# Optimization experiments

Hardware: AMD Instinct MI355X
Metric: run time of the kernel (lower is better)

Reference implementation:

```python
import jax, jax.numpy as jnp
import numpy as np

B, T, S = 32, 1000, 100
D, A, H, E, V, P = 512, 1024, 1024, 640, 10240, 1024
ZH, ZC = 0.05, 0.15  # zoneout factors (eval-mode deterministic blend)
NEG = -1e30


def setup_inputs() -> dict:
    key = jax.random.key(0)
    ks = jax.random.split(key, 20)
    w = lambda k, shape, s=0.02: jax.random.normal(k, shape, jnp.float32) * s
    return {
        "encoder_outputs": jax.random.normal(ks[0], (B, T, D), jnp.float32),
        "labels": jax.random.randint(ks[1], (B, S), 0, V),
        "enc_seq_len": jax.random.randint(ks[2], (B,), T // 2, T + 1).astype(jnp.int32),
        "embed": w(ks[3], (V, E)),
        "W_ih": w(ks[4], (4 * H, E + D)),
        "W_hh": w(ks[5], (4 * H, H)),
        "b_ih": jnp.zeros((4 * H,), jnp.float32),
        "b_hh": jnp.zeros((4 * H,), jnp.float32),
        "W_s": w(ks[6], (A, H)),
        "W_enc": w(ks[7], (A, D)),
        "b_enc": jnp.zeros((A,), jnp.float32),
        "v_att": w(ks[8], (1, A)),
        "W_fert": w(ks[9], (1, D)),
        "W_fb": w(ks[10], (A, 1)),
        "W_ro": w(ks[11], (P, H + E + D)),
        "b_ro": jnp.zeros((P,), jnp.float32),
        "W_out": w(ks[12], (V, P // 2)),
        "b_out": jnp.zeros((V,), jnp.float32),
    }


def _decoder(encoder_outputs, labels, enc_seq_len, embed, W_ih, W_hh, b_ih, b_hh,
             W_s, W_enc, b_enc, v_att, W_fert, W_fb, W_ro, b_ro, W_out, b_out):
    Bb, Tt, Dd = encoder_outputs.shape
    Hh = W_hh.shape[1]
    # shifted target embeddings (BOS = zeros): [B,S,E]
    emb = embed[labels]
    emb = jnp.pad(emb, ((0, 0), (1, 0), (0, 0)))[:, :-1, :]
    enc_ctx = jnp.einsum('btd,ad->bta', encoder_outputs, W_enc) + b_enc      # [B,T,A]
    inv_fert = jax.nn.sigmoid(jnp.einsum('btd,od->bto', encoder_outputs, W_fert))  # [B,T,1]
    mask = (jnp.arange(Tt)[None, :] < enc_seq_len[:, None])[:, :, None]      # [B,T,1]

    def step(carry, emb_t):
        h, c, att_ctx, accum = carry
        x = jnp.concatenate([emb_t, att_ctx], axis=-1)                       # [B,E+D]
        gates = x @ W_ih.T + b_ih + h @ W_hh.T + b_hh                        # [B,4H]
        i, f, g, o = jnp.split(gates, 4, axis=-1)
        c_new = jax.nn.sigmoid(f) * c + jax.nn.sigmoid(i) * jnp.tanh(g)
        h_new = jax.nn.sigmoid(o) * jnp.tanh(c_new)
        # zoneout (eval-mode expectation)
        h = ZH * h + (1.0 - ZH) * h_new
        c = ZC * c + (1.0 - ZC) * c_new
        s_t = h @ W_s.T                                                      # [B,A]
        fb = accum @ W_fb.T                                                  # [B,T,1]@[1,A] -> [B,T,A]
        energies = jnp.tanh(enc_ctx + s_t[:, None, :] + fb) @ v_att.T        # [B,T,1]
        energies = jnp.where(mask, energies, NEG)
        w_att = jax.nn.softmax(energies, axis=1)                             # [B,T,1]
        ctx = jnp.einsum('bt,btd->bd', w_att[..., 0], encoder_outputs)       # [B,D]
        accum = accum + w_att * inv_fert * 0.5
        return (h, c, ctx, accum), (h, ctx)

    zeros_h = jnp.zeros((Bb, Hh), encoder_outputs.dtype)
    carry0 = (zeros_h, zeros_h,
              jnp.zeros((Bb, Dd), encoder_outputs.dtype),
              jnp.zeros((Bb, Tt, 1), encoder_outputs.dtype))
    _, (s_seq, ctx_seq) = jax.lax.scan(step, carry0, jnp.swapaxes(emb, 0, 1))
    s_stk = jnp.swapaxes(s_seq, 0, 1)        # [B,S,H]
    ctx_stk = jnp.swapaxes(ctx_seq, 0, 1)    # [B,S,D]
    ro = jnp.concatenate([s_stk, emb, ctx_stk], axis=-1) @ W_ro.T + b_ro     # [B,S,P]
    ro = ro.reshape(ro.shape[0], ro.shape[1], -1, 2).max(axis=-1)            # MaxOut -> [B,S,P/2]
    logits = ro @ W_out.T + b_out                                            # [B,S,V]
    return logits


def reference(encoder_outputs, labels, enc_seq_len, embed, W_ih, W_hh, b_ih, b_hh,
              W_s, W_enc, b_enc, v_att, W_fert, W_fb, W_ro, b_ro, W_out, b_out):
    return _decoder(encoder_outputs, labels, enc_seq_len, embed, W_ih, W_hh, b_ih, b_hh,
                    W_s, W_enc, b_enc, v_att, W_fert, W_fb, W_ro, b_ro, W_out, b_out)
```

## Files before the change

### kernel.cpp

```cpp
#include <hip/hip_runtime.h>
#include <hip/hip_bf16.h>

typedef __bf16 bf16x8 __attribute__((ext_vector_type(8)));
typedef __bf16 bf16x4 __attribute__((ext_vector_type(4)));
typedef float  f32x4  __attribute__((ext_vector_type(4)));
typedef unsigned long long u64;

#define DI __device__ __forceinline__

DI float ex2f_(float x){ return __builtin_amdgcn_exp2f(x); }
DI float rcpf_(float x){ return __builtin_amdgcn_rcpf(x); }

DI u64 cload64(const void* p){
  return __hip_atomic_load((const u64*)p, __ATOMIC_RELAXED, __HIP_MEMORY_SCOPE_AGENT);
}
DI float cloadf(const float* p){
  return __hip_atomic_load(p, __ATOMIC_RELAXED, __HIP_MEMORY_SCOPE_AGENT);
}
DI void cstoreu(unsigned* p, unsigned v){
  __hip_atomic_store(p, v, __ATOMIC_RELAXED, __HIP_MEMORY_SCOPE_AGENT);
}
DI void cstoref(float* p, float v){
  __hip_atomic_store(p, v, __ATOMIC_RELAXED, __HIP_MEMORY_SCOPE_AGENT);
}

DI void bar_sync(unsigned* cnt, unsigned* flag, unsigned target){
  __syncthreads();
  if (threadIdx.x == 0){
    asm volatile("s_waitcnt vmcnt(0) lgkmcnt(0)" ::: "memory");
    __builtin_amdgcn_sched_barrier(0);
    unsigned old = __hip_atomic_fetch_add(cnt, 1u, __ATOMIC_RELAXED, __HIP_MEMORY_SCOPE_AGENT);
    if (old == target - 1u){
      __hip_atomic_store(flag, 1u, __ATOMIC_RELAXED, __HIP_MEMORY_SCOPE_AGENT);
    } else {
      while (__hip_atomic_load(flag, __ATOMIC_RELAXED, __HIP_MEMORY_SCOPE_AGENT) == 0u){
        __builtin_amdgcn_s_sleep(2);
      }
    }
    __builtin_amdgcn_sched_barrier(0);
  }
  __syncthreads();
}


__global__ void f32_to_bf16_k(const float* __restrict__ src, __bf16* __restrict__ dst, int n4){
  int i = blockIdx.x*256 + threadIdx.x;
  if (i >= n4) return;
  float4 v = reinterpret_cast<const float4*>(src)[i];
  bf16x4 o; o[0]=(__bf16)v.x; o[1]=(__bf16)v.y; o[2]=(__bf16)v.z; o[3]=(__bf16)v.w;
  reinterpret_cast<bf16x4*>(dst)[i] = o;
}

__global__ void emb_gather_k(const float* __restrict__ embed, const int* __restrict__ labels,
                             __bf16* __restrict__ out){
  int i = blockIdx.x*256 + threadIdx.x;
  if (i >= 100*32*80) return;
  int e8 = (i % 80)*8;
  int g  = i / 80;
  int b  = g & 31, s = g >> 5;
  bf16x8 o;
  if (s == 0){
    #pragma unroll
    for (int u=0;u<8;u++) o[u] = (__bf16)0.f;
  } else {
    int lbl = labels[b*100 + (s-1)];
    const float* pe = embed + (size_t)lbl*640 + e8;
    #pragma unroll
    for (int u=0;u<8;u++) o[u] = (__bf16)pe[u];
  }
  *reinterpret_cast<bf16x8*>(out + (size_t)g*640 + e8) = o;
}

__global__ __launch_bounds__(256) void fert_k(const float* __restrict__ enc,
                       const float* __restrict__ Wf, float* __restrict__ inv_fert){
  int row  = blockIdx.x*4 + (threadIdx.x>>6);
  int lane = threadIdx.x & 63;
  const float* pr = enc + (size_t)row*512 + lane*8;
  const float* pw = Wf + lane*8;
  float4 a0 = reinterpret_cast<const float4*>(pr)[0];
  float4 a1 = reinterpret_cast<const float4*>(pr)[1];
  float4 w0 = reinterpret_cast<const float4*>(pw)[0];
  float4 w1 = reinterpret_cast<const float4*>(pw)[1];
  float acc = a0.x*w0.x + a0.y*w0.y + a0.z*w0.z + a0.w*w0.w
            + a1.x*w1.x + a1.y*w1.y + a1.z*w1.z + a1.w*w1.w;
  #pragma unroll
  for (int off=1; off<64; off<<=1) acc += __shfl_xor(acc, off, 64);
  if (lane == 0) inv_fert[row] = 1.f/(1.f + expf(-acc));
}

__global__ void init_k(float* h, float* c, __bf16* hb, float* ctx_un, float* accum,
                       float* expe, float* sumb, unsigned* bars){
  int i = blockIdx.x*256 + threadIdx.x;
  if (i < 32768){ h[i]=0.f; c[i]=0.f; hb[i]=(__bf16)0.f; }
  if (i < 16384) ctx_un[i]=0.f;
  if (i < 32000) accum[i]=0.f;
  if (i < 64000) expe[i]=0.f;
  if (i < 64)    sumb[i]=1.f;
  if (i < 8192)  bars[i]=0u;
}

template<int MODE>
__global__ __launch_bounds__(256) void gemm_bt(const __bf16* __restrict__ A0,
        const __bf16* __restrict__ A1, const __bf16* __restrict__ A2,
        const __bf16* __restrict__ Bw, const float* __restrict__ bias,
        float* __restrict__ outF, __bf16* __restrict__ outB, int M, int N, int K){
  __shared__ __bf16 lA[64][40];
  __shared__ __bf16 lB[64][40];
  const int m0 = blockIdx.x*64, n0 = blockIdx.y*64;
  const int tid = threadIdx.x;
  const int wave = tid>>6, lane = tid&63;
  const int wm = wave>>1, wn = wave&1;
  const int srow = tid>>2, sc8 = (tid&3)*8;
  f32x4 acc[2][2];
  #pragma unroll
  for (int a=0;a<2;a++)
    #pragma unroll
    for (int b2=0;b2<2;b2++){ acc[a][b2][0]=0.f; acc[a][b2][1]=0.f; acc[a][b2][2]=0.f; acc[a][b2][3]=0.f; }

  for (int k0 = 0; k0 < K; k0 += 32){
    const int kk = k0 + sc8;
    bf16x8 av, bv;
    if (MODE == 1){
      const int m = m0 + srow;
      if (kk < 1024)      av = *reinterpret_cast<const bf16x8*>(A0 + (size_t)m*1024 + kk);
      else if (kk < 1664) av = *reinterpret_cast<const bf16x8*>(A1 + (size_t)m*640 + (kk-1024));
      else                av = *reinterpret_cast<const bf16x8*>(A2 + (size_t)m*512 + (kk-1664));
    } else {
      av = *reinterpret_cast<const bf16x8*>(A0 + (size_t)(m0+srow)*K + kk);
    }
    bv = *reinterpret_cast<const bf16x8*>(Bw + (size_t)(n0+srow)*K + kk);
    __syncthreads();
    *reinterpret_cast<bf16x8*>(&lA[srow][sc8]) = av;
    *reinterpret_cast<bf16x8*>(&lB[srow][sc8]) = bv;
    __syncthreads();
    #pragma unroll
    for (int mt=0;mt<2;mt++){
      bf16x8 af = *reinterpret_cast<const bf16x8*>(&lA[wm*32+mt*16+(lane&15)][(lane>>4)*8]);
      #pragma unroll
      for (int nt=0;nt<2;nt++){
        bf16x8 bf = *reinterpret_cast<const bf16x8*>(&lB[wn*32+nt*16+(lane&15)][(lane>>4)*8]);
        acc[mt][nt] = __builtin_amdgcn_mfma_f32_16x16x32_bf16(af, bf, acc[mt][nt], 0,0,0);
      }
    }
  }
  #pragma unroll
  for (int mt=0;mt<2;mt++){
    #pragma unroll
    for (int nt=0;nt<2;nt++){
      #pragma unroll
      for (int r=0;r<4;r++){
        const int m = m0 + wm*32 + mt*16 + (lane>>4)*4 + r;
        const int n = n0 + wn*32 + nt*16 + (lane&15);
        float v = acc[mt][nt][r] + bias[n];
        if (MODE == 0){
          outB[(size_t)m*N + n] = (__bf16)v;
        } else if (MODE == 1){
          float vo = fmaxf(v, __shfl_xor(v, 1, 64));
          if ((lane & 1) == 0) outB[(size_t)m*512 + (n>>1)] = (__bf16)vo;
        } else {
          const int rr = (m & 31)*100 + (m >> 5);
          outF[(size_t)rr*N + n] = v;
        }
      }
    }
  }
}

struct DecArgs {
  const float* b_ih; const float* b_hh;
  const float* v_att; const float* W_fb;
  const int* seqlen;
  const float* inv_fert;
  const __bf16* emb_sbe;
  const __bf16* W_ih_b; const __bf16* W_hh_b; const __bf16* W_s_b;
  const __bf16* enc_ctx; const __bf16* enc_b16;
  float* h_st; float* c_st; __bf16* h_b16;
  float* s_t; float* ctx_un; float* sum_buf;
  float* accum; float* expe;
  __bf16* s_stk; __bf16* ctx_stk;
  unsigned* bars;
};

struct SPd {
  __bf16 hA[32][1032];
  __bf16 cxA[32][520];
  float red[8][2][16][16];
  float gbuf[32][16];
  float sums[32];
};
struct SQd {
  __bf16 hb[1024];
  float st[1024];
  float she[128];
  float invp;
  float cred[8][516];
};

__global__ __launch_bounds__(512, 1) void decoder_kernel(DecArgs g){
  __shared__ __align__(16) char smem_raw[sizeof(SPd)];
  SPd& sp = *reinterpret_cast<SPd*>(smem_raw);
  SQd& sq = *reinterpret_cast<SQd*>(smem_raw);
  const int blk = blockIdx.x, tid = threadIdx.x;
  const int wave = tid>>6, lane = tid&63;
  const int bb = blk & 31, tc = blk >> 5;
  unsigned* bflag = g.bars + 4096;

  for (int s = 0; s < 100; ++s){
    const int p = s & 1, pp = 1 - p;

    {
      if (tid < 32) sp.sums[tid] = 1.f / cloadf(g.sum_buf + pp*32 + tid);
      __syncthreads();
      #pragma unroll
      for (int it = 0; it < 16; ++it){
        int i = tid + it*512;
        int row = i >> 8, c4 = (i & 255) * 4;
        *reinterpret_cast<u64*>(&sp.hA[row][c4]) = cload64(g.h_b16 + row*1024 + c4);
      }
      #pragma unroll
      for (int it = 0; it < 16; ++it){
        int i = tid + it*512;
        int row = i >> 8, c2 = (i & 255) * 2;
        u64 v = cload64(g.ctx_un + row*512 + c2);
        float2 f = __builtin_bit_cast(float2, v);
        float inv = sp.sums[row];
        __bf16 b0 = (__bf16)(f.x * inv), b1 = (__bf16)(f.y * inv);
        unsigned u = (unsigned)__builtin_bit_cast(unsigned short, b0)
                   | ((unsigned)__builtin_bit_cast(unsigned short, b1) << 16);
        *reinterpret_cast<unsigned*>(&sp.cxA[row][c2]) = u;
      }
      __syncthreads();

      const int j0 = blk*4;
      const int c = lane & 15, kg = lane >> 4;
      const int n = ((c>>2)<<10) + j0 + (c&3);
      const int brow0 = c, brow1 = c + 16;
      const int s0   = (wave<4) ? wave*9 : 36 + (wave-4)*8;
      const int scnt = (wave<4) ? 9 : 8;
      f32x4 acc0, acc1;
      acc0[0]=acc0[1]=acc0[2]=acc0[3]=0.f;
      acc1[0]=acc1[1]=acc1[2]=acc1[3]=0.f;
      const __bf16* embS = g.emb_sbe + (size_t)s*32*640;
      for (int ks = s0; ks < s0 + scnt; ++ks){
        const int kk = ks*32 + kg*8;
        bf16x8 bfrag = (kk < 1152)
          ? *reinterpret_cast<const bf16x8*>(g.W_ih_b + (size_t)n*1152 + kk)
          : *reinterpret_cast<const bf16x8*>(g.W_hh_b + (size_t)n*1024 + (kk-1152));
        bf16x8 a0, a1;
        if (kk < 640){
          a0 = *reinterpret_cast<const bf16x8*>(embS + brow0*640 + kk);
          a1 = *reinterpret_cast<const bf16x8*>(embS + brow1*640 + kk);
        } else if (kk < 1152){
          a0 = *reinterpret_cast<const bf16x8*>(&sp.cxA[brow0][kk-640]);
          a1 = *reinterpret_cast<const bf16x8*>(&sp.cxA[brow1][kk-640]);
        } else {
          a0 = *reinterpret_cast<const bf16x8*>(&sp.hA[brow0][kk-1152]);
          a1 = *reinterpret_cast<const bf16x8*>(&sp.hA[brow1][kk-1152]);
        }
        acc0 = __builtin_amdgcn_mfma_f32_16x16x32_bf16(a0, bfrag, acc0, 0,0,0);
        acc1 = __builtin_amdgcn_mfma_f32_16x16x32_bf16(a1, bfrag, acc1, 0,0,0);
      }
      #pragma unroll
      for (int r=0;r<4;r++){
        sp.red[wave][0][kg*4+r][c] = acc0[r];
        sp.red[wave][1][kg*4+r][c] = acc1[r];
      }
      __syncthreads();
      {
        const int mt = tid>>8, row = (tid>>4)&15, col = tid&15;
        float v = 0.f;
        #pragma unroll
        for (int w=0;w<8;w++) v += sp.red[w][mt][row][col];
        const int n2 = ((col>>2)<<10) + j0 + (col&3);
        sp.gbuf[mt*16+row][col] = v + g.b_ih[n2] + g.b_hh[n2];
      }
      __syncthreads();
      if (tid < 64){
        const int b = tid>>1, u = tid&1;
        unsigned packed = 0;
        #pragma unroll
        for (int d=0; d<2; ++d){
          const int cb = 2*u + d;
          const int j = j0 + cb;
          const float gi = sp.gbuf[b][cb],   gf = sp.gbuf[b][4+cb];
          const float gg = sp.gbuf[b][8+cb], go = sp.gbuf[b][12+cb];
          const float c_old = g.c_st[b*1024+j], h_old = g.h_st[b*1024+j];
          const float si = 1.f/(1.f+expf(-gi));
          const float sf = 1.f/(1.f+expf(-gf));
          const float so = 1.f/(1.f+expf(-go));
          const float cn = sf*c_old + si*tanhf(gg);
          const float hn = so*tanhf(cn);
          const float hz = 0.05f*h_old + 0.95f*hn;
          const float cz = 0.15f*c_old + 0.85f*cn;
          g.c_st[b*1024+j] = cz;
          g.h_st[b*1024+j] = hz;
          __bf16 hb = (__bf16)hz;
          packed |= ((unsigned)__builtin_bit_cast(unsigned short, hb)) << (16*d);
        }
        cstoreu(reinterpret_cast<unsigned*>(g.h_b16 + b*1024 + j0 + 2*u), packed);
        *reinterpret_cast<unsigned*>(g.s_stk + ((size_t)s*32+b)*1024 + j0 + 2*u) = packed;
      }
    }
    bar_sync(g.bars + s, bflag + s, 256);

    {
      if (tid < 256){
        *reinterpret_cast<u64*>(&sq.hb[tid*4]) = cload64(g.h_b16 + bb*1024 + tid*4);
      }
      if (tid == 500) sq.invp = 1.f / cloadf(g.sum_buf + pp*32 + bb);
      __syncthreads();
      const float invp = sq.invp;
      {
        const int a = tc*128 + (tid>>2), kc = tid&3;
        const __bf16* wr = g.W_s_b + (size_t)a*1024 + kc*256;
        const __bf16* hr = &sq.hb[kc*256];
        float acc = 0.f;
        #pragma unroll
        for (int i=0;i<32;i++){
          bf16x8 w8 = *reinterpret_cast<const bf16x8*>(wr + i*8);
          bf16x8 h8 = *reinterpret_cast<const bf16x8*>(hr + i*8);
          #pragma unroll
          for (int u2=0;u2<8;u2++) acc = fmaf((float)w8[u2], (float)h8[u2], acc);
        }
        acc += __shfl_xor(acc, 1, 64);
        acc += __shfl_xor(acc, 2, 64);
        if (kc == 0) cstoref(g.s_t + bb*1024 + a, acc);
      }
      if (tid < 64){
        const int d = tc*64 + tid;
        if (s > 0){
          const float cv = cloadf(g.ctx_un + bb*512 + d);
          g.ctx_stk[((size_t)(s-1)*32+bb)*512 + d] = (__bf16)(cv * invp);
        }
        cstoref(g.ctx_un + bb*512 + d, 0.f);
      }
      if (tid < 125){
        const int t = tc*125 + tid, idx = bb*1000 + t;
        g.accum[idx] = fmaf(g.expe[pp*32000+idx]*g.inv_fert[idx], 0.5f*invp, g.accum[idx]);
      }
      if (tid == 501 && tc == 0) cstoref(g.sum_buf + p*32 + bb, 0.f);
    }
    bar_sync(g.bars + 200 + s*32 + bb, bflag + 200 + s*32 + bb, 8);

    {
      const int t_base = tc*125;
      *reinterpret_cast<u64*>(&sq.st[tid*2]) = cload64(g.s_t + bb*1024 + tid*2);
      __syncthreads();
      const int len_b = g.seqlen[bb];
      float sv[16], v2[16], wf[16];
      float vbase = 0.f;
      #pragma unroll
      for (int half=0; half<2; ++half){
        const int a0i = half*512 + lane*8;
        const float4 sA = *reinterpret_cast<const float4*>(&sq.st[a0i]);
        const float4 sB = *reinterpret_cast<const float4*>(&sq.st[a0i+4]);
        const float4 vA = *reinterpret_cast<const float4*>(g.v_att + a0i);
        const float4 vB = *reinterpret_cast<const float4*>(g.v_att + a0i + 4);
        const float4 fA = *reinterpret_cast<const float4*>(g.W_fb + a0i);
        const float4 fB = *reinterpret_cast<const float4*>(g.W_fb + a0i + 4);
        sv[half*8+0]=sA.x; sv[half*8+1]=sA.y; sv[half*8+2]=sA.z; sv[half*8+3]=sA.w;
        sv[half*8+4]=sB.x; sv[half*8+5]=sB.y; sv[half*8+6]=sB.z; sv[half*8+7]=sB.w;
        wf[half*8+0]=fA.x; wf[half*8+1]=fA.y; wf[half*8+2]=fA.z; wf[half*8+3]=fA.w;
        wf[half*8+4]=fB.x; wf[half*8+5]=fB.y; wf[half*8+6]=fB.z; wf[half*8+7]=fB.w;
        v2[half*8+0]=-2.f*vA.x; v2[half*8+1]=-2.f*vA.y; v2[half*8+2]=-2.f*vA.z; v2[half*8+3]=-2.f*vA.w;
        v2[half*8+4]=-2.f*vB.x; v2[half*8+5]=-2.f*vB.y; v2[half*8+6]=-2.f*vB.z; v2[half*8+7]=-2.f*vB.w;
        vbase += vA.x+vA.y+vA.z+vA.w+vB.x+vB.y+vB.z+vB.w;
      }
      float wsum = 0.f;
      {
        const __bf16* ebase = g.enc_ctx + ((size_t)bb*1000)*1024 + lane*8;
        const int nIter = (wave < 5) ? 16 : 15;
        int t = t_base + wave;
        bf16x8 curA = *reinterpret_cast<const bf16x8*>(ebase + (size_t)t*1024);
        bf16x8 curB = *reinterpret_cast<const bf16x8*>(ebase + (size_t)t*1024 + 512);
        for (int k = 0; k < nIter; ++k){
          const int tn = t + 8;
          bf16x8 nxtA = curA, nxtB = curB;
          if (k + 1 < nIter){
            nxtA = *reinterpret_cast<const bf16x8*>(ebase + (size_t)tn*1024);
            nxtB = *reinterpret_cast<const bf16x8*>(ebase + (size_t)tn*1024 + 512);
          }
          const int idx = bb*1000 + t;
          float px = 0.f;
          if (t < len_b){
            const float ac = g.accum[idx];
            float e = vbase;
            #pragma unroll
            for (int u=0;u<8;u++){
              const float z = fmaf(ac, wf[u], sv[u] + (float)curA[u]);
              e = fmaf(v2[u], rcpf_(ex2f_(z * 2.885390082f) + 1.f), e);
            }
            #pragma unroll
            for (int u=0;u<8;u++){
              const float z = fmaf(ac, wf[8+u], sv[8+u] + (float)curB[u]);
              e = fmaf(v2[8+u], rcpf_(ex2f_(z * 2.885390082f) + 1.f), e);
            }
            #pragma unroll
            for (int off=1; off<64; off<<=1) e += __shfl_xor(e, off, 64);
            px = ex2f_(e * 1.44269504f);
          }
          if (lane == 0){
            g.expe[p*32000 + idx] = px;
            sq.she[t - t_base] = px;
          }
          wsum += px;
          curA = nxtA; curB = nxtB;
          t = tn;
        }
      }
      if (lane == 0) atomicAdd(g.sum_buf + p*32 + bb, wsum);
      __syncthreads();
      {
        const int d8 = (tid & 63) * 8;
        const int tt = wave;
        float cacc[8];
        #pragma unroll
        for (int u=0;u<8;u++) cacc[u] = 0.f;
        const __bf16* vb = g.enc_b16 + ((size_t)bb*1000)*512 + d8;
        const int nI2 = (tt < 5) ? 16 : 15;
        int t2 = t_base + tt;
        #pragma unroll 4
        for (int k = 0; k < nI2; ++k){
          const float w = sq.she[t2 - t_base];
          const bf16x8 ev = *reinterpret_cast<const bf16x8*>(vb + (size_t)t2*512);
          #pragma unroll
          for (int u=0;u<8;u++) cacc[u] = fmaf(w, (float)ev[u], cacc[u]);
          t2 += 8;
        }
        #pragma unroll
        for (int u=0;u<8;u++) sq.cred[tt][d8+u] = cacc[u];
        __syncthreads();
        const int d = tid & 511;
        float ssum = 0.f;
        #pragma unroll
        for (int w8=0; w8<8; ++w8) ssum += sq.cred[w8][d];
        atomicAdd(g.ctx_un + bb*512 + d, ssum);
      }
    }
    bar_sync(g.bars + 100 + s, bflag + 100 + s, 256);
  }

  if (tid < 64){
    const int d = tc*64 + tid;
    const float invp = 1.f / cloadf(g.sum_buf + 32 + bb);
    const float cv = cloadf(g.ctx_un + bb*512 + d);
    g.ctx_stk[((size_t)99*32 + bb)*512 + d] = (__bf16)(cv * invp);
  }
}

extern "C" void kernel_launch(void* const* d_in, const int* in_sizes, int n_in,
                              void* d_out, int out_size, void* d_ws, size_t ws_size,
                              hipStream_t stream){
  (void)in_sizes; (void)n_in; (void)out_size; (void)ws_size;
  const float* enc    = (const float*)d_in[0];
  const int*   labels = (const int*)  d_in[1];
  const int*   seqlen = (const int*)  d_in[2];
  const float* embed  = (const float*)d_in[3];
  const float* W_ih   = (const float*)d_in[4];
  const float* W_hh   = (const float*)d_in[5];
  const float* b_ih   = (const float*)d_in[6];
  const float* b_hh   = (const float*)d_in[7];
  const float* W_s    = (const float*)d_in[8];
  const float* W_enc  = (const float*)d_in[9];
  const float* b_enc  = (const float*)d_in[10];
  const float* v_att  = (const float*)d_in[11];
  const float* W_fert = (const float*)d_in[12];
  const float* W_fb   = (const float*)d_in[13];
  const float* W_ro   = (const float*)d_in[14];
  const float* b_ro   = (const float*)d_in[15];
  const float* W_out  = (const float*)d_in[16];
  const float* b_out  = (const float*)d_in[17];
  float* out = (float*)d_out;

  char* ws = (char*)d_ws;
  size_t off = 0;
  auto alloc = [&](size_t bytes)->char*{
    char* p = ws + off;
    off = (off + bytes + 255) & ~(size_t)255;
    return p;
  };
  __bf16* enc_b16 = (__bf16*)alloc(32000ull*512*2);
  __bf16* enc_ctx = (__bf16*)alloc(32000ull*1024*2);
  __bf16* W_ih_b  = (__bf16*)alloc(4096ull*1152*2);
  __bf16* W_hh_b  = (__bf16*)alloc(4096ull*1024*2);
  __bf16* W_s_b   = (__bf16*)alloc(1024ull*1024*2);
  __bf16* W_enc_b = (__bf16*)alloc(1024ull*512*2);
  __bf16* W_ro_b  = (__bf16*)alloc(1024ull*2176*2);
  __bf16* W_out_b = (__bf16*)alloc(10240ull*512*2);
  __bf16* emb_sbe = (__bf16*)alloc(3200ull*640*2);
  float*  ifert   = (float*)alloc(32000ull*4);
  __bf16* s_stk   = (__bf16*)alloc(3200ull*1024*2);
  __bf16* ctx_stk = (__bf16*)alloc(3200ull*512*2);
  float*  h_st    = (float*)alloc(32768ull*4);
  float*  c_st    = (float*)alloc(32768ull*4);
  __bf16* h_b16   = (__bf16*)alloc(32768ull*2);
  float*  s_t     = (float*)alloc(32768ull*4);
  float*  ctx_un  = (float*)alloc(16384ull*4);
  float*  sum_buf = (float*)alloc(256);
  float*  accum   = (float*)alloc(32000ull*4);
  float*  expe    = (float*)alloc(64000ull*4);
  __bf16* Y       = (__bf16*)alloc(3200ull*512*2);
  unsigned* bars  = (unsigned*)alloc(8192ull*4);

  auto conv = [&](const float* s, __bf16* d, int n){
    int n4 = n/4;
    f32_to_bf16_k<<<(n4+255)/256, 256, 0, stream>>>(s, d, n4);
  };
  conv(enc,   enc_b16, 32000*512);
  conv(W_ih,  W_ih_b,  4096*1152);
  conv(W_hh,  W_hh_b,  4096*1024);
  conv(W_s,   W_s_b,   1024*1024);
  conv(W_enc, W_enc_b, 1024*512);
  conv(W_ro,  W_ro_b,  1024*2176);
  conv(W_out, W_out_b, 10240*512);

  emb_gather_k<<<(256000+255)/256, 256, 0, stream>>>(embed, labels, emb_sbe);
  fert_k<<<8000, 256, 0, stream>>>(enc, W_fert, ifert);
  init_k<<<250, 256, 0, stream>>>(h_st, c_st, h_b16, ctx_un, accum, expe, sum_buf, bars);

  gemm_bt<0><<<dim3(500,16), 256, 0, stream>>>(enc_b16, nullptr, nullptr, W_enc_b,
        b_enc, nullptr, enc_ctx, 32000, 1024, 512);

  DecArgs da;
  da.b_ih = b_ih; da.b_hh = b_hh; da.v_att = v_att; da.W_fb = W_fb;
  da.seqlen = seqlen; da.inv_fert = ifert;
  da.emb_sbe = emb_sbe; da.W_ih_b = W_ih_b; da.W_hh_b = W_hh_b; da.W_s_b = W_s_b;
  da.enc_ctx = enc_ctx; da.enc_b16 = enc_b16;
  da.h_st = h_st; da.c_st = c_st; da.h_b16 = h_b16;
  da.s_t = s_t; da.ctx_un = ctx_un; da.sum_buf = sum_buf;
  da.accum = accum; da.expe = expe;
  da.s_stk = s_stk; da.ctx_stk = ctx_stk;
  da.bars = bars;
  void* kargs[] = { &da };
  hipLaunchCooperativeKernel(reinterpret_cast<void*>(decoder_kernel),
                             dim3(256), dim3(512), kargs, 0, stream);

  gemm_bt<1><<<dim3(50,16), 256, 0, stream>>>(s_stk, emb_sbe, ctx_stk, W_ro_b,
        b_ro, nullptr, Y, 3200, 1024, 2176);
  gemm_bt<2><<<dim3(50,160), 256, 0, stream>>>(Y, nullptr, nullptr, W_out_b,
        b_out, out, nullptr, 3200, 10240, 512);
}
```

Baseline: 7.266 ms.

## Keep encoder attention context resident in registers across decoder steps

Loads this block's slice of enc_ctx (16 timesteps × 16 bf16 per lane) into registers once before the 100-step loop, instead of streaming it from global memory every step. The attention-score loop is fully unrolled and reads from these registers. It also changes launch_bounds minBlocks from 1 to 2. That limits registers per thread, while the new 128-register-wide cache adds pressure, so spilling is a real risk.

```diff
diff --git a/kernel.cpp b/kernel.cpp
--- a/kernel.cpp
+++ b/kernel.cpp
@@ -196,14 +196,28 @@
   float cred[8][516];
 };
 
-__global__ __launch_bounds__(512, 1) void decoder_kernel(DecArgs g){
+__global__ __launch_bounds__(512, 2) void decoder_kernel(DecArgs g){
   __shared__ __align__(16) char smem_raw[sizeof(SPd)];
   SPd& sp = *reinterpret_cast<SPd*>(smem_raw);
   SQd& sq = *reinterpret_cast<SQd*>(smem_raw);
   const int blk = blockIdx.x, tid = threadIdx.x;
   const int wave = tid>>6, lane = tid&63;
   const int bb = blk & 31, tc = blk >> 5;
+  const int t_base = tc*125;
   unsigned* bflag = g.bars + 4096;
+
+  bf16x8 ecr[16][2];
+  {
+    const __bf16* ebase = g.enc_ctx + ((size_t)bb*1000)*1024 + lane*8;
+    const int nIter = (wave < 5) ? 16 : 15;
+    #pragma unroll
+    for (int k = 0; k < 16; ++k){
+      int t = t_base + wave + 8*k;
+      if (k >= nIter) t = t_base + wave;
+      ecr[k][0] = *reinterpret_cast<const bf16x8*>(ebase + (size_t)t*1024);
+      ecr[k][1] = *reinterpret_cast<const bf16x8*>(ebase + (size_t)t*1024 + 512);
+    }
+  }
 
   for (int s = 0; s < 100; ++s){
     const int p = s & 1, pp = 1 - p;
@@ -343,7 +357,6 @@
     bar_sync(g.bars + 200 + s*32 + bb, bflag + 200 + s*32 + bb, 8);
 
     {
-      const int t_base = tc*125;
       *reinterpret_cast<u64*>(&sq.st[tid*2]) = cload64(g.s_t + bb*1024 + tid*2);
       __syncthreads();
       const int len_b = g.seqlen[bb];
@@ -368,44 +381,36 @@
       }
       float wsum = 0.f;
       {
-        const __bf16* ebase = g.enc_ctx + ((size_t)bb*1000)*1024 + lane*8;
         const int nIter = (wave < 5) ? 16 : 15;
-        int t = t_base + wave;
-        bf16x8 curA = *reinterpret_cast<const bf16x8*>(ebase + (size_t)t*1024);
-        bf16x8 curB = *reinterpret_cast<const bf16x8*>(ebase + (size_t)t*1024 + 512);
-        for (int k = 0; k < nIter; ++k){
-          const int tn = t + 8;
-          bf16x8 nxtA = curA, nxtB = curB;
-          if (k + 1 < nIter){
-            nxtA = *reinterpret_cast<const bf16x8*>(ebase + (size_t)tn*1024);
-            nxtB = *reinterpret_cast<const bf16x8*>(ebase + (size_t)tn*1024 + 512);
+        #pragma unroll
+        for (int k = 0; k < 16; ++k){
+          if (k < nIter){
+            const int t = t_base + wave + 8*k;
+            const int idx = bb*1000 + t;
+            float px = 0.f;
+            if (t < len_b){
+              const float ac = g.accum[idx];
+              float e = vbase;
+              #pragma unroll
+              for (int u=0;u<8;u++){
+                const float z = fmaf(ac, wf[u], sv[u] + (float)ecr[k][0][u]);
+                e = fmaf(v2[u], rcpf_(ex2f_(z * 2.885390082f) + 1.f), e);
+              }
+              #pragma unroll
+              for (int u=0;u<8;u++){
+                const float z = fmaf(ac, wf[8+u], sv[8+u] + (float)ecr[k][1][u]);
+                e = fmaf(v2[8+u], rcpf_(ex2f_(z * 2.885390082f) + 1.f), e);
+              }
+              #pragma unroll
+              for (int off=1; off<64; off<<=1) e += __shfl_xor(e, off, 64);
+              px = ex2f_(e * 1.44269504f);
+            }
+            if (lane == 0){
+              g.expe[p*32000 + idx] = px;
+              sq.she[t - t_base] = px;
+            }
+            wsum += px;
           }
-          const int idx = bb*1000 + t;
-          float px = 0.f;
-          if (t < len_b){
-            const float ac = g.accum[idx];
-            float e = vbase;
-            #pragma unroll
-            for (int u=0;u<8;u++){
-              const float z = fmaf(ac, wf[u], sv[u] + (float)curA[u]);
-              e = fmaf(v2[u], rcpf_(ex2f_(z * 2.885390082f) + 1.f), e);
-            }
-            #pragma unroll
-            for (int u=0;u<8;u++){
-              const float z = fmaf(ac, wf[8+u], sv[8+u] + (float)curB[u]);
-              e = fmaf(v2[8+u], rcpf_(ex2f_(z * 2.885390082f) + 1.f), e);
-            }
-            #pragma unroll
-            for (int off=1; off<64; off<<=1) e += __shfl_xor(e, off, 64);
-            px = ex2f_(e * 1.44269504f);
-          }
-          if (lane == 0){
-            g.expe[p*32000 + idx] = px;
-            sq.she[t - t_base] = px;
-          }
-          wsum += px;
-          curA = nxtA; curB = nxtB;
-          t = tn;
         }
       }
       if (lane == 0) atomicAdd(g.sum_buf + p*32 + bb, wsum);
```

Result: slower. 12.98 ms (+78.6%).
